# Performance work log

Hardware: AMD Instinct MI355X
Metric: run time of the kernel (lower is better)

## Reference

```python
import jax, jax.numpy as jnp
import numpy as np

N_NODES = 100000
N_EDGES = 3200000
DIN, DHID, DOUT = 128, 128, 128


def setup_inputs() -> dict:
    key = jax.random.key(0)
    ks = jax.random.split(key, 8)
    x = jax.random.normal(ks[0], (N_NODES, DIN), dtype=jnp.float32)
    edge_index = jax.random.randint(ks[1], (2, N_EDGES), 0, N_NODES, dtype=jnp.int32)
    def glorot(k, fan_in, fan_out):
        s = jnp.sqrt(6.0 / (fan_in + fan_out)).astype(jnp.float32)
        return jax.random.uniform(k, (fan_in, fan_out), jnp.float32, -s, s)
    return {
        "x": x,
        "edge_index": edge_index,
        "w1": glorot(ks[2], DIN, DHID), "b1": jnp.zeros((DHID,), jnp.float32),
        "w2": glorot(ks[3], DHID, DHID), "b2": jnp.zeros((DHID,), jnp.float32),
        "w3": glorot(ks[4], DHID, DOUT), "b3": jnp.zeros((DOUT,), jnp.float32),
    }


def reference(x, edge_index, w1, b1, w2, b2, w3, b3):
    n = x.shape[0]
    # GCN normalization with self-loops (PyG gcn_norm, edge_weight = 1)
    loop = jnp.arange(n, dtype=edge_index.dtype)
    src = jnp.concatenate([edge_index[0], loop])  # [E+N]
    dst = jnp.concatenate([edge_index[1], loop])  # [E+N]
    deg = jax.ops.segment_sum(jnp.ones_like(dst, dtype=x.dtype), dst, num_segments=n)
    dinv = jnp.where(deg > 0, jax.lax.rsqrt(deg), 0.0)
    norm = dinv[src] * dinv[dst]  # [E+N]

    def gcn_conv(h, w, b):
        h = h @ w  # [N, dout]
        msg = norm[:, None] * h[src]  # gather + scale, [E+N, dout]
        agg = jax.ops.segment_sum(msg, dst, num_segments=n)  # scatter-add
        return agg + b

    h = jax.nn.relu(gcn_conv(x, w1, b1))
    h = jax.nn.relu(gcn_conv(h, w2, b2))  # dropout p=0 / eval: no-op
    h = gcn_conv(h, w3, b3)
    return jnp.sum(h, axis=0, keepdims=True) / h.shape[0]  # [1, DOUT]
```

## Files before the change

### kernel.cpp

```cpp
#include <hip/hip_runtime.h>

#define D 128
#define BSH 8
#define CAP 12288
#define CH 8192

typedef unsigned short ushort_t;
typedef unsigned int uint_t;
typedef unsigned char uchar_t;

typedef __attribute__((ext_vector_type(8))) short frag_ab;
typedef __attribute__((ext_vector_type(4))) float frag_cd;
typedef __attribute__((ext_vector_type(2))) float float2v;

union frag_u { ushort_t u[8]; frag_ab v; };


__device__ __forceinline__ float bf2f(ushort_t u) {
    union { uint_t i; float f; } v; v.i = ((uint_t)u) << 16; return v.f;
}
__device__ __forceinline__ ushort_t f2bf(float f) {
    union { float f; uint_t i; } v; v.f = f;
    uint_t u = v.i;
    u += 0x7fffu + ((u >> 16) & 1u);
    return (ushort_t)(u >> 16);
}

__device__ __forceinline__ void acc_fp8(uint_t w, float2v& aA, float2v& aB) {
    aA += __builtin_amdgcn_cvt_pk_f32_fp8(w, false);
    aB += __builtin_amdgcn_cvt_pk_f32_fp8(w, true);
}
__device__ __forceinline__ uint_t g8(const uint_t* __restrict__ t8, uint_t byteoff) {
    return *(const uint_t*)((const char*)t8 + byteoff);
}

__launch_bounds__(512)
__global__ void k_binpack(const int* __restrict__ src, const int* __restrict__ dst,
                          int* __restrict__ curA, int* __restrict__ curB,
                          uint_t* __restrict__ binA, uint_t* __restrict__ binB,
                          int E, int nb, int nbin,
                          const float* __restrict__ W1, const float* __restrict__ W2,
                          ushort_t* __restrict__ h1, ushort_t* __restrict__ l1,
                          ushort_t* __restrict__ h2, ushort_t* __restrict__ l2,
                          const float* __restrict__ b1, const float* __restrict__ b2,
                          float* __restrict__ bp1, float* __restrict__ bp2,
                          uint_t* __restrict__ zrow) {
    int tx = threadIdx.x;

    if (blockIdx.x >= nbin) {
        int wb = blockIdx.x - nbin;
        if (wb == 64) {
            if (tx < 128) {
                int c = (tx & 7) * 16 + (tx >> 3);
                bp1[tx] = b1[c];
                bp2[tx] = b2[c];
            }
            if (tx >= 128 && tx < 160) zrow[tx - 128] = 0;
            return;
        }
        int gid = wb * 512 + tx;
        int which = gid >> 14;
        int idx = gid & 16383;
        int k = idx >> 7, n = idx & 127;
        float w = which ? W2[(((k & 7) * 16) + (k >> 3)) * 128 + n] : W1[idx];
        ushort_t h = f2bf(w);
        ushort_t l = f2bf(w - bf2f(h));
        int c = k >> 5, quad = (k >> 3) & 3, jj = k & 7;
        int j = n >> 4, l16 = n & 15;
        int lane = quad * 16 + l16;
        int dest = ((c * 8 + j) * 64 + lane) * 8 + jj;
        if (which) { h2[dest] = h; l2[dest] = l; }
        else       { h1[dest] = h; l1[dest] = l; }
        return;
    }

    __shared__ int hA[512], hB[512], sc[512], gb[512];
    __shared__ ushort_t sbkt[CH];
    __shared__ uint_t sent[CH];
    hA[tx] = 0; hB[tx] = 0;
    __syncthreads();

    int e0 = blockIdx.x * CH;
    int e1 = min(e0 + CH, E);
    int total = e1 - e0;

    int sreg[16], dreg[16];
#pragma unroll
    for (int it = 0; it < 16; ++it) {
        int e = e0 + tx + it * 512;
        if (e < e1) {
            int s = src[e], d = dst[e];
            sreg[it] = s; dreg[it] = d;
            atomicAdd(&hA[d >> BSH], 1);
            atomicAdd(&hB[s >> BSH], 1);
        }
    }
    __syncthreads();

    {
        int v = hA[tx];
        sc[tx] = v;
        __syncthreads();
        for (int d = 1; d < 512; d <<= 1) {
            int t = (tx >= d) ? sc[tx - d] : 0;
            __syncthreads();
            sc[tx] += t;
            __syncthreads();
        }
        sc[tx] -= v;
        gb[tx] = v ? atomicAdd(&curA[tx], v) : 0;
        hA[tx] = 0;
        __syncthreads();
#pragma unroll
        for (int it = 0; it < 16; ++it) {
            int e = e0 + tx + it * 512;
            if (e < e1) {
                int s = sreg[it], d = dreg[it];
                int k = d >> BSH;
                int pos = sc[k] + atomicAdd(&hA[k], 1);
                sent[pos] = ((uint_t)s << 8) | (uint_t)(d & 255);
                sbkt[pos] = (ushort_t)k;
            }
        }
        __syncthreads();
        for (int p = tx; p < total; p += 512) {
            int k = sbkt[p];
            int gp = gb[k] + (p - sc[k]);
            if (gp < CAP) binA[(size_t)k * CAP + gp] = sent[p];
        }
        __syncthreads();
    }

    {
        int v = hB[tx];
        sc[tx] = v;
        __syncthreads();
        for (int d = 1; d < 512; d <<= 1) {
            int t = (tx >= d) ? sc[tx - d] : 0;
            __syncthreads();
            sc[tx] += t;
            __syncthreads();
        }
        sc[tx] -= v;
        gb[tx] = v ? atomicAdd(&curB[tx], v) : 0;
        hB[tx] = 0;
        __syncthreads();
#pragma unroll
        for (int it = 0; it < 16; ++it) {
            int e = e0 + tx + it * 512;
            if (e < e1) {
                int s = sreg[it], d = dreg[it];
                int k = s >> BSH;
                int pos = sc[k] + atomicAdd(&hB[k], 1);
                sent[pos] = ((uint_t)d << 8) | (uint_t)(s & 255);
                sbkt[pos] = (ushort_t)k;
            }
        }
        __syncthreads();
        for (int p = tx; p < total; p += 512) {
            int k = sbkt[p];
            int gp = gb[k] + (p - sc[k]);
            if (gp < CAP) binB[(size_t)k * CAP + gp] = sent[p];
        }
    }
}

__launch_bounds__(1024)
__global__ void k_csr(const uint_t* __restrict__ binA, const int* __restrict__ curA,
                      float* __restrict__ dinv, int* __restrict__ row_beg,
                      int* __restrict__ row_end, int* __restrict__ csr_src, int N) {
    __shared__ int hist[256];
    __shared__ int scan[256];
    __shared__ uint_t ebuf[CAP];
    int b = blockIdx.x;
    int tx = threadIdx.x;
    int cnt = min(curA[b], CAP);
    const uint_t* eb = binA + (size_t)b * CAP;

    if (tx < 256) hist[tx] = 0;
    __syncthreads();
    for (int e = tx; e < cnt; e += 1024) {
        uint_t pk = eb[e];
        ebuf[e] = pk;
        atomicAdd(&hist[pk & 255u], 1);
    }
    __syncthreads();
    int v = 0, pd = 0;
    if (tx < 256) {
        v = hist[tx];
        pd = (v + 15) & ~15;
        scan[tx] = pd;
    }
    __syncthreads();
    for (int dd = 1; dd < 256; dd <<= 1) {
        int t = 0;
        if (tx < 256 && tx >= dd) t = scan[tx - dd];
        __syncthreads();
        if (tx < 256) scan[tx] += t;
        __syncthreads();
    }
    if (tx < 256) {
        int my_excl = scan[tx] - pd;
        int node = b * 256 + tx;
        if (node < N) {
            dinv[node] = rsqrtf((float)(v + 1));
            row_beg[node] = b * CAP + my_excl;
            row_end[node] = b * CAP + my_excl + pd;
        }
        for (int i = v; i < pd; i++)
            csr_src[b * CAP + my_excl + i] = N;
        hist[tx] = my_excl;
    }
    __syncthreads();
    for (int e = tx; e < cnt; e += 1024) {
        uint_t pk = ebuf[e];
        int pos = b * CAP + atomicAdd(&hist[pk & 255u], 1);
        csr_src[pos] = (int)(pk >> 8);
    }
}

template <int IN_F32>
__launch_bounds__(256)
__global__ void gemm_mfma(const void* __restrict__ Av, const ushort_t* __restrict__ Whi,
                          const ushort_t* __restrict__ Wlo, const float* __restrict__ dinv,
                          uchar_t* __restrict__ C8, int nrows, int gemm_blocks,
                          const uint_t* __restrict__ binB, const int* __restrict__ curB,
                          float* __restrict__ ow) {
    __shared__ float owacc[256];
    if ((int)blockIdx.x >= gemm_blocks) {
        int b = blockIdx.x - gemm_blocks;
        int tx = threadIdx.x;
        owacc[tx] = 0.f;
        __syncthreads();
        int cnt = min(curB[b], CAP);
        const uint_t* eb = binB + (size_t)b * CAP;
        for (int e = tx; e < cnt; e += 256) {
            uint_t pk = eb[e];
            atomicAdd(&owacc[pk & 255u], dinv[pk >> 8]);
        }
        __syncthreads();
        ow[b * 256 + tx] = owacc[tx];
        return;
    }

    int wave = threadIdx.x >> 6;
    int lane = threadIdx.x & 63;
    int quad = lane >> 4, l16 = lane & 15;
    int base = blockIdx.x * 128 + wave * 32;

    frag_cd acc[2][8];
#pragma unroll
    for (int rt = 0; rt < 2; rt++)
#pragma unroll
        for (int j = 0; j < 8; j++) acc[rt][j] = (frag_cd)0.f;

    const ushort_t* Ab = (const ushort_t*)Av;
    const float* Af = (const float*)Av;

#pragma unroll
    for (int c = 0; c < 4; c++) {
        frag_ab afrag[2];
        int koff = c * 32 + quad * 8;
#pragma unroll
        for (int rt = 0; rt < 2; rt++) {
            int row = min(base + rt * 16 + l16, nrows - 1);
            if (IN_F32) {
                const float* ap = Af + (size_t)row * D + koff;
                float4 a0 = *(const float4*)ap;
                float4 a1 = *(const float4*)(ap + 4);
                frag_u fu;
                fu.u[0] = f2bf(a0.x); fu.u[1] = f2bf(a0.y);
                fu.u[2] = f2bf(a0.z); fu.u[3] = f2bf(a0.w);
                fu.u[4] = f2bf(a1.x); fu.u[5] = f2bf(a1.y);
                fu.u[6] = f2bf(a1.z); fu.u[7] = f2bf(a1.w);
                afrag[rt] = fu.v;
            } else {
                afrag[rt] = *(const frag_ab*)(Ab + (size_t)row * D + koff);
            }
        }
#pragma unroll
        for (int j = 0; j < 8; j++) {
            frag_ab bh = *(const frag_ab*)(Whi + (((c * 8 + j) * 64 + lane) * 8));
            frag_ab bl = *(const frag_ab*)(Wlo + (((c * 8 + j) * 64 + lane) * 8));
#pragma unroll
            for (int rt = 0; rt < 2; rt++) {
                acc[rt][j] = __builtin_amdgcn_mfma_f32_16x16x32_bf16(afrag[rt], bh,
                                                                     acc[rt][j], 0, 0, 0);
                acc[rt][j] = __builtin_amdgcn_mfma_f32_16x16x32_bf16(afrag[rt], bl,
                                                                     acc[rt][j], 0, 0, 0);
            }
        }
    }

#pragma unroll
    for (int rt = 0; rt < 2; rt++) {
        int rbase = base + rt * 16 + quad * 4;
#pragma unroll
        for (int reg = 0; reg < 4; reg++) {
            int row = rbase + reg;
            if (row < nrows) {
                float dv = dinv[row];
                uint_t d0 = (uint_t)__builtin_amdgcn_cvt_pk_fp8_f32(
                    acc[rt][0][reg] * dv, acc[rt][1][reg] * dv, 0, false);
                d0 = (uint_t)__builtin_amdgcn_cvt_pk_fp8_f32(
                    acc[rt][2][reg] * dv, acc[rt][3][reg] * dv, (int)d0, true);
                uint_t d1 = (uint_t)__builtin_amdgcn_cvt_pk_fp8_f32(
                    acc[rt][4][reg] * dv, acc[rt][5][reg] * dv, 0, false);
                d1 = (uint_t)__builtin_amdgcn_cvt_pk_fp8_f32(
                    acc[rt][6][reg] * dv, acc[rt][7][reg] * dv, (int)d1, true);
                uint2 o; o.x = d0; o.y = d1;
                *(uint2*)(C8 + (size_t)row * D + l16 * 8) = o;
            }
        }
    }
}

__launch_bounds__(256)
__global__ void agg8(const uint_t* __restrict__ t8, const int* __restrict__ csr_src,
                     const int* __restrict__ row_beg, const int* __restrict__ row_end,
                     const float* __restrict__ dinv, const float* __restrict__ bias,
                     uint_t* __restrict__ out, int n, int do_relu) {
    int node = blockIdx.x * 4 + (threadIdx.x >> 6);
    if (node >= n) return;
    int lane = threadIdx.x & 63;
    int eh = lane >> 5;
    uint_t cl = (uint_t)(lane & 31);
    uint_t cl4 = cl * 4u;

    int beg = row_beg[node];
    int cnt = row_end[node] - beg;
    float dn = dinv[node];

    float2v accA = {0.f, 0.f}, accB = {0.f, 0.f};

    if (eh == 0) {
        uint_t w = g8(t8, (uint_t)node * 128u + cl4);
        accA = __builtin_amdgcn_cvt_pk_f32_fp8(w, false);
        accB = __builtin_amdgcn_cvt_pk_f32_fp8(w, true);
    }

    int half = cnt >> 1;
    int e     = beg + (eh ? half : 0);
    int nfull = half >> 3;

    uint4 sa, sb;
    if (nfull > 0) {
        __builtin_memcpy(&sa, csr_src + e, 16);
        __builtin_memcpy(&sb, csr_src + e + 4, 16);
    }
    for (int it = 0; it < nfull; ++it) {
        uint4 ca = sa, cb = sb;
        e += 8;
        if (it + 1 < nfull) {
            __builtin_memcpy(&sa, csr_src + e, 16);
            __builtin_memcpy(&sb, csr_src + e + 4, 16);
        }
        uint_t w0 = g8(t8, ca.x * 128u + cl4);
        uint_t w1 = g8(t8, ca.y * 128u + cl4);
        uint_t w2 = g8(t8, ca.z * 128u + cl4);
        uint_t w3 = g8(t8, ca.w * 128u + cl4);
        uint_t w4 = g8(t8, cb.x * 128u + cl4);
        uint_t w5 = g8(t8, cb.y * 128u + cl4);
        uint_t w6 = g8(t8, cb.z * 128u + cl4);
        uint_t w7 = g8(t8, cb.w * 128u + cl4);
        acc_fp8(w0, accA, accB);
        acc_fp8(w1, accA, accB);
        acc_fp8(w2, accA, accB);
        acc_fp8(w3, accA, accB);
        acc_fp8(w4, accA, accB);
        acc_fp8(w5, accA, accB);
        acc_fp8(w6, accA, accB);
        acc_fp8(w7, accA, accB);
    }

    float a0 = accA.x, a1 = accA.y, a2 = accB.x, a3 = accB.y;
    a0 += __shfl(a0, lane ^ 32, 64);
    a1 += __shfl(a1, lane ^ 32, 64);
    a2 += __shfl(a2, lane ^ 32, 64);
    a3 += __shfl(a3, lane ^ 32, 64);

    if (eh == 0) {
        float4 bb = ((const float4*)bias)[cl];
        float o0 = dn * a0 + bb.x;
        float o1 = dn * a1 + bb.y;
        float o2 = dn * a2 + bb.z;
        float o3 = dn * a3 + bb.w;
        if (do_relu) {
            o0 = fmaxf(o0, 0.f); o1 = fmaxf(o1, 0.f);
            o2 = fmaxf(o2, 0.f); o3 = fmaxf(o3, 0.f);
        }
        uint2 ow;
        ow.x = (uint_t)f2bf(o0) | ((uint_t)f2bf(o1) << 16);
        ow.y = (uint_t)f2bf(o2) | ((uint_t)f2bf(o3) << 16);
        ((uint2*)out)[(size_t)node * 32 + cl] = ow;
    }
}

__launch_bounds__(512)
__global__ void wreduce2(const ushort_t* __restrict__ h, const float* __restrict__ ow,
                         const float* __restrict__ dinv, float* __restrict__ vpart,
                         int n) {
    __shared__ float s[512];
    int bx = blockIdx.x;
    int tx = threadIdx.x;
    int c = tx & 127;
    int rg = tx >> 7;
    int base = bx * 128;
    int lim = min(base + 128, n);
    float acc = 0.f;
    for (int r = base + rg; r < lim; r += 4) {
        float dv = dinv[r];
        float cv = dv * (dv + ow[r]);
        acc += cv * bf2f(h[(size_t)r * D + c]);
    }
    s[tx] = acc;
    __syncthreads();
    if (tx < 128)
        vpart[(size_t)bx * 128 + tx] =
            (s[tx] + s[tx + 128]) + (s[tx + 256] + s[tx + 384]);
}

__launch_bounds__(512)
__global__ void finalize2(const float* __restrict__ vpart, int nparts,
                          const float* __restrict__ w3, const float* __restrict__ b3,
                          float* __restrict__ out, float invn) {
    __shared__ float s[512];
    __shared__ float sv[D];
    int tx = threadIdx.x;
    int c = tx & 127;
    int rg = tx >> 7;
    float acc = 0.f;
    for (int p = rg; p < nparts; p += 4)
        acc += vpart[(size_t)p * 128 + c];
    s[tx] = acc;
    __syncthreads();
    if (tx < 128)
        sv[tx] = (s[tx] + s[tx + 128]) + (s[tx + 256] + s[tx + 384]);
    __syncthreads();
    if (tx < 128) {
        float f2 = 0.f;
        for (int k = 0; k < D; k++) {
            int p = (k & 15) * 8 + (k >> 4);
            f2 += sv[p] * w3[(size_t)k * D + tx];
        }
        out[tx] = f2 * invn + b3[tx];
    }
}

extern "C" void kernel_launch(void* const* d_in, const int* in_sizes, int n_in,
                              void* d_out, int out_size, void* d_ws, size_t ws_size,
                              hipStream_t stream) {
    const float* x   = (const float*)d_in[0];
    const int*   ei  = (const int*)d_in[1];
    const float* w1  = (const float*)d_in[2];
    const float* b1  = (const float*)d_in[3];
    const float* w2  = (const float*)d_in[4];
    const float* b2  = (const float*)d_in[5];
    const float* w3  = (const float*)d_in[6];
    const float* b3  = (const float*)d_in[7];
    float* out = (float*)d_out;

    const int N = in_sizes[0] / D;
    const int E = in_sizes[1] / 2;
    const int* src = ei;
    const int* dst = ei + E;
    const int nb = (N + 255) >> 8;
    const int nbin = (E + CH - 1) / CH;
    const int nw2 = (N + 127) >> 7;

    char* p = (char*)d_ws;
    auto alloc = [&](size_t bytes) -> char* {
        char* r = p;
        p += (bytes + 255) & ~(size_t)255;
        return r;
    };
    char*     zbeg     = p;
    int*      curA     = (int*)alloc(512 * 4);
    int*      curB     = (int*)alloc(512 * 4);
    char*     zend     = p;
    float*    ow       = (float*)alloc((size_t)nb * 256 * 4);
    float*    vpart    = (float*)alloc((size_t)nw2 * 128 * 4);
    float*    dinv     = (float*)alloc((size_t)N * 4);
    int*      row_beg  = (int*)alloc((size_t)N * 4);
    int*      row_end  = (int*)alloc((size_t)N * 4);
    ushort_t* wp1h     = (ushort_t*)alloc(16384 * 2);
    ushort_t* wp1l     = (ushort_t*)alloc(16384 * 2);
    ushort_t* wp2h     = (ushort_t*)alloc(16384 * 2);
    ushort_t* wp2l     = (ushort_t*)alloc(16384 * 2);
    float*    bp1      = (float*)alloc(D * 4);
    float*    bp2      = (float*)alloc(D * 4);
    uint_t*   binA     = (uint_t*)alloc((size_t)nb * CAP * 4);
    uint_t*   binB     = (uint_t*)alloc((size_t)nb * CAP * 4);
    int*      csr_src  = (int*)alloc((size_t)nb * CAP * 4);
    ushort_t* bufH     = (ushort_t*)alloc((size_t)N * D * 2);
    uint_t*   buf8     = (uint_t*)alloc((size_t)(N + 1) * 32 * 4);
    (void)ws_size;

    const int gG = (N + 127) / 128;

    hipMemsetAsync(zbeg, 0, (size_t)(zend - zbeg), stream);

    k_binpack<<<nbin + 65, 512, 0, stream>>>(src, dst, curA, curB, binA, binB, E, nb,
                                             nbin, w1, w2, wp1h, wp1l, wp2h, wp2l,
                                             b1, b2, bp1, bp2, buf8 + (size_t)N * 32);
    k_csr<<<nb, 1024, 0, stream>>>(binA, curA, dinv, row_beg, row_end, csr_src, N);

    gemm_mfma<1><<<gG + nb, 256, 0, stream>>>(x, wp1h, wp1l, dinv, (uchar_t*)buf8, N,
                                              gG, binB, curB, ow);
    agg8<<<(N + 3) / 4, 256, 0, stream>>>(buf8, csr_src, row_beg, row_end, dinv, bp1,
                                          (uint_t*)bufH, N, 1);
    gemm_mfma<0><<<gG, 256, 0, stream>>>(bufH, wp2h, wp2l, dinv, (uchar_t*)buf8, N,
                                         gG, binB, curB, ow);
    agg8<<<(N + 3) / 4, 256, 0, stream>>>(buf8, csr_src, row_beg, row_end, dinv, bp2,
                                          (uint_t*)bufH, N, 1);
    wreduce2<<<nw2, 512, 0, stream>>>(bufH, ow, dinv, vpart, N);
    finalize2<<<1, 512, 0, stream>>>(vpart, nw2, w3, b3, out, 1.0f / (float)N);
}
```

Measured before the change: 396.5 us.

## Stage GEMM weights in LDS and split reduction accumulators for ILP

The MFMA GEMM kernel now copies both bf16 weight halves (64 KB) into shared memory once per block and reads B fragments from LDS instead of global memory. The wreduce2 and finalize2 kernels use multiple independent accumulators to expose more memory-level parallelism. The LDS staging adds a 64 KB allocation per block, which limits occupancy, and a sync plus copy cost per block. The bin-count blocks that share the kernel also reserve this larger LDS.

Measured after the change: 343.3 us. 1.15x faster.

```diff
diff --git a/kernel.cpp b/kernel.cpp
--- a/kernel.cpp
+++ b/kernel.cpp
@@ -226,10 +226,12 @@
                           uchar_t* __restrict__ C8, int nrows, int gemm_blocks,
                           const uint_t* __restrict__ binB, const int* __restrict__ curB,
                           float* __restrict__ ow) {
-    __shared__ float owacc[256];
+    __shared__ ushort_t sW[32768];
+    int tx = threadIdx.x;
+
     if ((int)blockIdx.x >= gemm_blocks) {
+        float* owacc = (float*)sW;
         int b = blockIdx.x - gemm_blocks;
-        int tx = threadIdx.x;
         owacc[tx] = 0.f;
         __syncthreads();
         int cnt = min(curB[b], CAP);
@@ -243,8 +245,19 @@
         return;
     }
 
-    int wave = threadIdx.x >> 6;
-    int lane = threadIdx.x & 63;
+    {
+        uint4* dW = (uint4*)sW;
+        const uint4* sH = (const uint4*)Whi;
+        const uint4* sL = (const uint4*)Wlo;
+        for (int i = tx; i < 2048; i += 256) {
+            dW[i] = sH[i];
+            dW[i + 2048] = sL[i];
+        }
+    }
+    __syncthreads();
+
+    int wave = tx >> 6;
+    int lane = tx & 63;
     int quad = lane >> 4, l16 = lane & 15;
     int base = blockIdx.x * 128 + wave * 32;
 
@@ -280,8 +293,9 @@
         }
 #pragma unroll
         for (int j = 0; j < 8; j++) {
-            frag_ab bh = *(const frag_ab*)(Whi + (((c * 8 + j) * 64 + lane) * 8));
-            frag_ab bl = *(const frag_ab*)(Wlo + (((c * 8 + j) * 64 + lane) * 8));
+            int boff = ((c * 8 + j) * 64 + lane) * 8;
+            frag_ab bh = *(const frag_ab*)(sW + boff);
+            frag_ab bl = *(const frag_ab*)(sW + 16384 + boff);
 #pragma unroll
             for (int rt = 0; rt < 2; rt++) {
                 acc[rt][j] = __builtin_amdgcn_mfma_f32_16x16x32_bf16(afrag[rt], bh,
@@ -407,13 +421,23 @@
     int rg = tx >> 7;
     int base = bx * 128;
     int lim = min(base + 128, n);
-    float acc = 0.f;
-    for (int r = base + rg; r < lim; r += 4) {
-        float dv = dinv[r];
-        float cv = dv * (dv + ow[r]);
-        acc += cv * bf2f(h[(size_t)r * D + c]);
-    }
-    s[tx] = acc;
+    float acc0 = 0.f, acc1 = 0.f;
+    int r = base + rg;
+    for (; r + 4 < lim; r += 8) {
+        float dv0 = dinv[r];
+        float cv0 = dv0 * (dv0 + ow[r]);
+        acc0 += cv0 * bf2f(h[(size_t)r * D + c]);
+        int r1 = r + 4;
+        float dv1 = dinv[r1];
+        float cv1 = dv1 * (dv1 + ow[r1]);
+        acc1 += cv1 * bf2f(h[(size_t)r1 * D + c]);
+    }
+    if (r < lim) {
+        float dv0 = dinv[r];
+        float cv0 = dv0 * (dv0 + ow[r]);
+        acc0 += cv0 * bf2f(h[(size_t)r * D + c]);
+    }
+    s[tx] = acc0 + acc1;
     __syncthreads();
     if (tx < 128)
         vpart[(size_t)bx * 128 + tx] =
@@ -429,21 +453,40 @@
     int tx = threadIdx.x;
     int c = tx & 127;
     int rg = tx >> 7;
-    float acc = 0.f;
-    for (int p = rg; p < nparts; p += 4)
-        acc += vpart[(size_t)p * 128 + c];
-    s[tx] = acc;
+    float a0 = 0.f, a1 = 0.f, a2 = 0.f, a3 = 0.f;
+    float a4 = 0.f, a5 = 0.f, a6 = 0.f, a7 = 0.f;
+    int p = rg;
+    for (; p + 28 < nparts; p += 32) {
+        a0 += vpart[(size_t)(p)      * 128 + c];
+        a1 += vpart[(size_t)(p +  4) * 128 + c];
+        a2 += vpart[(size_t)(p +  8) * 128 + c];
+        a3 += vpart[(size_t)(p + 12) * 128 + c];
+        a4 += vpart[(size_t)(p + 16) * 128 + c];
+        a5 += vpart[(size_t)(p + 20) * 128 + c];
+        a6 += vpart[(size_t)(p + 24) * 128 + c];
+        a7 += vpart[(size_t)(p + 28) * 128 + c];
+    }
+    for (; p < nparts; p += 4) a0 += vpart[(size_t)p * 128 + c];
+    s[tx] = ((a0 + a1) + (a2 + a3)) + ((a4 + a5) + (a6 + a7));
     __syncthreads();
     if (tx < 128)
         sv[tx] = (s[tx] + s[tx + 128]) + (s[tx + 256] + s[tx + 384]);
     __syncthreads();
     if (tx < 128) {
-        float f2 = 0.f;
-        for (int k = 0; k < D; k++) {
-            int p = (k & 15) * 8 + (k >> 4);
-            f2 += sv[p] * w3[(size_t)k * D + tx];
-        }
-        out[tx] = f2 * invn + b3[tx];
+        float f0 = 0.f, f1 = 0.f, f2 = 0.f, f3 = 0.f;
+        float f4 = 0.f, f5 = 0.f, f6 = 0.f, f7 = 0.f;
+        for (int k0 = 0; k0 < D; k0 += 8) {
+            f0 += sv[((k0    ) & 15) * 8 + ((k0    ) >> 4)] * w3[(size_t)(k0    ) * D + tx];
+            f1 += sv[((k0 + 1) & 15) * 8 + ((k0 + 1) >> 4)] * w3[(size_t)(k0 + 1) * D + tx];
+            f2 += sv[((k0 + 2) & 15) * 8 + ((k0 + 2) >> 4)] * w3[(size_t)(k0 + 2) * D + tx];
+            f3 += sv[((k0 + 3) & 15) * 8 + ((k0 + 3) >> 4)] * w3[(size_t)(k0 + 3) * D + tx];
+            f4 += sv[((k0 + 4) & 15) * 8 + ((k0 + 4) >> 4)] * w3[(size_t)(k0 + 4) * D + tx];
+            f5 += sv[((k0 + 5) & 15) * 8 + ((k0 + 5) >> 4)] * w3[(size_t)(k0 + 5) * D + tx];
+            f6 += sv[((k0 + 6) & 15) * 8 + ((k0 + 6) >> 4)] * w3[(size_t)(k0 + 6) * D + tx];
+            f7 += sv[((k0 + 7) & 15) * 8 + ((k0 + 7) >> 4)] * w3[(size_t)(k0 + 7) * D + tx];
+        }
+        float f = ((f0 + f1) + (f2 + f3)) + ((f4 + f5) + (f6 + f7));
+        out[tx] = f * invn + b3[tx];
     }
 }
 
```
